# Kernel tuning notes

Hardware: AMD Instinct MI355X
Metric: run time of the kernel (lower is better)

The kernel has to match this reference:

```python
import jax, jax.numpy as jnp
import numpy as np

H = 16        # query heads
KV = 4        # key/value heads
HD = 64       # head dim
BASE = 10000.0
SCALE = HD ** (-0.5) * 0.8


def setup_inputs() -> dict:
    key = jax.random.key(0)
    ks = jax.random.split(key, 5)
    B, S, D = 2, 4096, 1024
    return {
        "hidden_states": jax.random.normal(ks[0], (B, S, D), dtype=jnp.float32),
        "wq": jax.random.normal(ks[1], (D, H * HD), dtype=jnp.float32) * (D ** -0.5),
        "wk": jax.random.normal(ks[2], (D, KV * HD), dtype=jnp.float32) * (D ** -0.5),
        "wv": jax.random.normal(ks[3], (D, KV * HD), dtype=jnp.float32) * (D ** -0.5),
        "wo": jax.random.normal(ks[4], (H * HD, D), dtype=jnp.float32) * ((H * HD) ** -0.5),
    }


def _rope_tables(seq_len, dtype):
    inv_freq = 1.0 / (BASE ** (jnp.arange(0, HD, 2, dtype=jnp.float32) / HD))
    t = jnp.arange(seq_len, dtype=jnp.float32)
    freqs = t[:, None] * inv_freq[None, :]            # [S, HD/2]
    emb = jnp.concatenate([freqs, freqs], axis=-1)    # [S, HD]
    return jnp.cos(emb).astype(dtype), jnp.sin(emb).astype(dtype)


def _rotate_half(x):
    x1, x2 = x[..., : HD // 2], x[..., HD // 2 :]
    return jnp.concatenate([-x2, x1], axis=-1)


def reference(hidden_states, wq, wk, wv, wo):
    B, S, D = hidden_states.shape
    G = H // KV
    q = (hidden_states @ wq).reshape(B, S, H, HD).transpose(0, 2, 1, 3)   # [B,H,S,HD]
    k = (hidden_states @ wk).reshape(B, S, KV, HD).transpose(0, 2, 1, 3)  # [B,KV,S,HD]
    v = (hidden_states @ wv).reshape(B, S, KV, HD).transpose(0, 2, 1, 3)
    cos, sin = _rope_tables(S, q.dtype)               # [S,HD] each
    cos = cos[None, None]                             # [1,1,S,HD]
    sin = sin[None, None]
    q = q * cos + _rotate_half(q) * sin
    k = k * cos + _rotate_half(k) * sin
    k = jnp.repeat(k, G, axis=1)                      # [B,H,S,HD]
    v = jnp.repeat(v, G, axis=1)
    scores = jnp.einsum("bhqd,bhkd->bhqk", q, k) * SCALE
    probs = jax.nn.softmax(scores.astype(jnp.float32), axis=-1).astype(q.dtype)
    out = jnp.einsum("bhqk,bhkd->bhqd", probs, v)     # [B,H,S,HD]
    out = out.transpose(0, 2, 1, 3).reshape(B, S, H * HD)
    return out @ wo
```

## Files before the change

### kernel.cpp

```cpp
#include <hip/hip_runtime.h>
#include <hip/hip_fp16.h>
#include <math.h>

typedef _Float16 f16;
typedef _Float16 half8 __attribute__((ext_vector_type(8)));
typedef _Float16 half4v __attribute__((ext_vector_type(4)));
typedef _Float16 half2v __attribute__((ext_vector_type(2)));
typedef float f32x4 __attribute__((ext_vector_type(4)));
typedef float f32x16 __attribute__((ext_vector_type(16)));
typedef unsigned uint2v __attribute__((ext_vector_type(2)));

#define NB 2
#define NS 4096
#define ND 1024
#define NH 16
#define NKV 4
#define NHD 64
#define ATT_SCALE2 0.14426950408889634f

__global__ __launch_bounds__(256) void wprep_k(
    const float* __restrict__ wq, const float* __restrict__ wk,
    const float* __restrict__ wv, const float* __restrict__ wo,
    f16* __restrict__ Bt, f16* __restrict__ Wot)
{
  __shared__ f16 tile[64][72];
  int bx = blockIdx.x, by = blockIdx.y;
  const float* src; int ldn, colbase, nbase; f16* dst;
  if (bx < 24) {
    int n0 = bx * 64;
    if (n0 < 1024)      { src = wq; ldn = 1024; colbase = n0; }
    else if (n0 < 1280) { src = wk; ldn = 256;  colbase = n0 - 1024; }
    else                { src = wv; ldn = 256;  colbase = n0 - 1280; }
    dst = Bt; nbase = n0;
  } else {
    src = wo; ldn = 1024; colbase = (bx - 24) * 64; dst = Wot; nbase = (bx - 24) * 64;
  }
  int tid = threadIdx.x;
  int kr = tid >> 4;
  int nc = (tid & 15) * 4;
  #pragma unroll
  for (int i = 0; i < 4; ++i) {
    int k = by * 64 + kr + i * 16;
    float4 v = *reinterpret_cast<const float4*>(src + (size_t)k * ldn + colbase + nc);
    tile[nc + 0][kr + i * 16] = (f16)v.x;
    tile[nc + 1][kr + i * 16] = (f16)v.y;
    tile[nc + 2][kr + i * 16] = (f16)v.z;
    tile[nc + 3][kr + i * 16] = (f16)v.w;
  }
  __syncthreads();
  int nl = tid >> 2;
  int kb = (tid & 3) * 16;
  half8 a = *reinterpret_cast<const half8*>(&tile[nl][kb]);
  half8 b = *reinterpret_cast<const half8*>(&tile[nl][kb + 8]);
  f16* o = dst + (size_t)(nbase + nl) * 1024 + by * 64 + kb;
  *reinterpret_cast<half8*>(o) = a;
  *reinterpret_cast<half8*>(o + 8) = b;
}

template<int MODE>
__global__ __launch_bounds__(256) void gemm_k(
    const float* __restrict__ Af32, const f16* __restrict__ Af16,
    const f16* __restrict__ Bt,
    f16* __restrict__ q_h, f16* __restrict__ k_h, f16* __restrict__ vT_h,
    float* __restrict__ outp)
{
  __shared__ f16 As[128 * 32];
  __shared__ f16 Bs[128 * 32];
  int tid = threadIdx.x;
  int lane = tid & 63, w = tid >> 6;
  int wr = w >> 1, wc = w & 1;
  int g = lane >> 4, lr = lane & 15;
  int m0 = blockIdx.y * 128, n0 = blockIdx.x * 128;

  f32x4 acc[4][4] = {};

  int ar = tid >> 1;
  int ac = (tid & 1) * 16;

  for (int k0 = 0; k0 < ND; k0 += 32) {
    if (MODE == 0) {
      const float* Ap = Af32 + (size_t)(m0 + ar) * ND + k0 + ac;
      #pragma unroll
      for (int i = 0; i < 4; ++i) {
        float4 v = *reinterpret_cast<const float4*>(Ap + i * 4);
        int col = ac + i * 4;
        int slot = (col >> 3) ^ (ar & 3);
        half4v hv = { (f16)v.x, (f16)v.y, (f16)v.z, (f16)v.w };
        *reinterpret_cast<half4v*>(&As[ar * 32 + slot * 8 + (col & 7)]) = hv;
      }
    } else {
      const f16* Ap = Af16 + (size_t)(m0 + ar) * ND + k0 + ac;
      half8 v0 = *reinterpret_cast<const half8*>(Ap);
      half8 v1 = *reinterpret_cast<const half8*>(Ap + 8);
      int s0 = (ac >> 3) ^ (ar & 3);
      int s1 = ((ac >> 3) + 1) ^ (ar & 3);
      *reinterpret_cast<half8*>(&As[ar * 32 + s0 * 8]) = v0;
      *reinterpret_cast<half8*>(&As[ar * 32 + s1 * 8]) = v1;
    }
    {
      const f16* Bp = Bt + (size_t)(n0 + ar) * ND + k0 + ac;
      half8 v0 = *reinterpret_cast<const half8*>(Bp);
      half8 v1 = *reinterpret_cast<const half8*>(Bp + 8);
      int s0 = (ac >> 3) ^ (ar & 3);
      int s1 = ((ac >> 3) + 1) ^ (ar & 3);
      *reinterpret_cast<half8*>(&Bs[ar * 32 + s0 * 8]) = v0;
      *reinterpret_cast<half8*>(&Bs[ar * 32 + s1 * 8]) = v1;
    }
    __syncthreads();
    half8 af[4], bf[4];
    #pragma unroll
    for (int mt = 0; mt < 4; ++mt) {
      int row = wr * 64 + mt * 16 + lr;
      af[mt] = *reinterpret_cast<const half8*>(&As[row * 32 + (g ^ (row & 3)) * 8]);
    }
    #pragma unroll
    for (int nt = 0; nt < 4; ++nt) {
      int row = wc * 64 + nt * 16 + lr;
      bf[nt] = *reinterpret_cast<const half8*>(&Bs[row * 32 + (g ^ (row & 3)) * 8]);
    }
    #pragma unroll
    for (int mt = 0; mt < 4; ++mt)
      #pragma unroll
      for (int nt = 0; nt < 4; ++nt)
        acc[mt][nt] = __builtin_amdgcn_mfma_f32_16x16x32_f16(af[mt], bf[nt], acc[mt][nt], 0, 0, 0);
    __syncthreads();
  }

  #pragma unroll
  for (int mt = 0; mt < 4; ++mt)
    #pragma unroll
    for (int nt = 0; nt < 4; ++nt)
      #pragma unroll
      for (int r = 0; r < 4; ++r) {
        int m = m0 + wr * 64 + mt * 16 + g * 4 + r;
        int n = n0 + wc * 64 + nt * 16 + lr;
        float val = acc[mt][nt][r];
        if (MODE == 0) {
          int b = m >> 12, s = m & (NS - 1);
          f16 hv = (f16)val;
          if (n < 1024)      q_h[(((size_t)b * NH + (n >> 6)) * NS + s) * NHD + (n & 63)] = hv;
          else if (n < 1280) { int nn = n - 1024; k_h[(((size_t)b * NKV + (nn >> 6)) * NS + s) * NHD + (nn & 63)] = hv; }
          else               { int nn = n - 1280; vT_h[(((size_t)b * NKV + (nn >> 6)) * NHD + (nn & 63)) * NS + s] = hv; }
        } else {
          outp[(size_t)m * ND + n] = val;
        }
      }
}

__global__ __launch_bounds__(256) void rope_k(f16* __restrict__ q_h, f16* __restrict__ k_h)
{
  __shared__ float cs[16][33], sn[16][33];
  int b = blockIdx.y;
  int s0 = blockIdx.x * 16;
  int tid = threadIdx.x;
  for (int idx = tid; idx < 512; idx += 256) {
    int sl = idx >> 5, d = idx & 31;
    double inv = exp((double)d * -0.28782313662425575);
    double ang = (double)(s0 + sl) * inv;
    cs[sl][d] = (float)cos(ang);
    sn[sl][d] = (float)sin(ang);
  }
  __syncthreads();
  for (int p = tid; p < 512 * 20; p += 256) {
    int u = p >> 9; int rem = p & 511; int sl = rem >> 5; int d = rem & 31;
    f16* ptr;
    if (u < NH) ptr = q_h + (((size_t)b * NH + u) * NS + s0 + sl) * NHD;
    else        ptr = k_h + (((size_t)b * NKV + (u - NH)) * NS + s0 + sl) * NHD;
    float x1 = (float)ptr[d], x2 = (float)ptr[d + 32];
    float c = cs[sl][d], si = sn[sl][d];
    ptr[d]      = (f16)(x1 * c - x2 * si);
    ptr[d + 32] = (f16)(x2 * c + x1 * si);
  }
}

__global__ __launch_bounds__(512) void attn_k(
    const f16* __restrict__ q_h, const f16* __restrict__ k_h,
    const f16* __restrict__ vT_h, f16* __restrict__ attn_h)
{
  __shared__ f16 Ks[2][64 * 64];
  __shared__ f16 Vs[2][64 * 64];
  int tid = threadIdx.x;
  int lane = tid & 63, w = tid >> 6;
  int hi = lane >> 5, qr = lane & 31;
  int bh = blockIdx.x; int b = bh >> 4, h = bh & 15, kvh = h >> 2;
  int q0 = blockIdx.y * 256 + w * 32;

  const f16* qptr = q_h + (((size_t)b * NH + h) * NS + q0 + qr) * NHD + hi * 8;
  half8 qf[4];
  #pragma unroll
  for (int ks = 0; ks < 4; ++ks)
    qf[ks] = *reinterpret_cast<const half8*>(qptr + 16 * ks);

  const f16* kbase = k_h + ((size_t)b * NKV + kvh) * NS * NHD;
  const f16* vbase = vT_h + ((size_t)b * NKV + kvh) * NHD * NS;

  f32x16 accO[2] = {};
  float m_run = -1e30f;
  float l_lane = 0.f;

  int srow = tid >> 3;
  int scol = (tid & 7) * 8;
  int sslot = ((scol >> 3) ^ (srow & 7)) * 8;
  int qs = qr & 7;

  {
    half8 kv0 = *reinterpret_cast<const half8*>(kbase + (size_t)srow * NHD + scol);
    half8 vv0 = *reinterpret_cast<const half8*>(vbase + (size_t)srow * NS + scol);
    *reinterpret_cast<half8*>(&Ks[0][srow * 64 + sslot]) = kv0;
    *reinterpret_cast<half8*>(&Vs[0][srow * 64 + sslot]) = vv0;
  }

  const half2v ones2 = { (f16)1.0f, (f16)1.0f };

  int cur = 0;
  for (int t = 0; t < 64; ++t) {
    __syncthreads();
    int tn = (t < 63) ? t + 1 : t;
    int kt2 = tn * 64;
    half8 kreg = *reinterpret_cast<const half8*>(kbase + (size_t)(kt2 + srow) * NHD + scol);
    half8 vreg = *reinterpret_cast<const half8*>(vbase + (size_t)srow * NS + kt2 + scol);

    const f16* Kc = &Ks[cur][0];
    const f16* Vc = &Vs[cur][0];

    f32x16 sc0 = {}, sc1 = {};
    #pragma unroll
    for (int ks = 0; ks < 4; ++ks) {
      int cs = 2 * ks + hi;
      half8 kf0 = *reinterpret_cast<const half8*>(&Kc[qr * 64 + ((cs ^ qs) << 3)]);
      half8 kf1 = *reinterpret_cast<const half8*>(&Kc[(32 + qr) * 64 + ((cs ^ qs) << 3)]);
      __builtin_amdgcn_s_setprio(1);
      sc0 = __builtin_amdgcn_mfma_f32_32x32x16_f16(kf0, qf[ks], sc0, 0, 0, 0);
      sc1 = __builtin_amdgcn_mfma_f32_32x32x16_f16(kf1, qf[ks], sc1, 0, 0, 0);
      __builtin_amdgcn_s_setprio(0);
    }

    float mx = sc0[0];
    #pragma unroll
    for (int i = 1; i < 16; ++i) mx = fmaxf(mx, sc0[i]);
    #pragma unroll
    for (int i = 0; i < 16; ++i) mx = fmaxf(mx, sc1[i]);
    float mxs = mx * ATT_SCALE2;

    if (__any(mxs > m_run + 8.0f)) {
      float mw = fmaxf(mxs, __shfl_xor(mxs, 32));
      float mnew = fmaxf(m_run, mw);
      float alpha = exp2f(m_run - mnew);
      #pragma unroll
      for (int db = 0; db < 2; ++db)
        #pragma unroll
        for (int i = 0; i < 16; ++i) accO[db][i] *= alpha;
      l_lane *= alpha;
      m_run = mnew;
    }

    unsigned wrd[2][4][2];
    float l0 = 0.f, l1 = 0.f;
    #pragma unroll
    for (int e = 0; e < 4; ++e)
      #pragma unroll
      for (int p = 0; p < 2; ++p) {
        float a0 = exp2f(fmaf(sc0[e * 4 + p * 2], ATT_SCALE2, -m_run));
        float a1 = exp2f(fmaf(sc0[e * 4 + p * 2 + 1], ATT_SCALE2, -m_run));
        unsigned u0 = __builtin_bit_cast(unsigned, __builtin_amdgcn_cvt_pkrtz(a0, a1));
        wrd[0][e][p] = u0;
        l0 = __builtin_amdgcn_fdot2(__builtin_bit_cast(half2v, u0), ones2, l0, false);
        float b0 = exp2f(fmaf(sc1[e * 4 + p * 2], ATT_SCALE2, -m_run));
        float b1 = exp2f(fmaf(sc1[e * 4 + p * 2 + 1], ATT_SCALE2, -m_run));
        unsigned u1 = __builtin_bit_cast(unsigned, __builtin_amdgcn_cvt_pkrtz(b0, b1));
        wrd[1][e][p] = u1;
        l1 = __builtin_amdgcn_fdot2(__builtin_bit_cast(half2v, u1), ones2, l1, false);
      }
    l_lane += l0 + l1;

    #pragma unroll
    for (int ks = 0; ks < 4; ++ks) {
      int kb = ks >> 1, e0 = 2 * (ks & 1);
      uint2v s0 = __builtin_amdgcn_permlane32_swap(wrd[kb][e0][0], wrd[kb][e0 + 1][0], false, false);
      uint2v s1 = __builtin_amdgcn_permlane32_swap(wrd[kb][e0][1], wrd[kb][e0 + 1][1], false, false);
      union { unsigned u[4]; half8 h; } pfu;
      pfu.u[0] = s0[0]; pfu.u[1] = s1[0]; pfu.u[2] = s0[1]; pfu.u[3] = s1[1];
      int cs = 2 * ks + hi;
      half8 vf0 = *reinterpret_cast<const half8*>(&Vc[qr * 64 + ((cs ^ qs) << 3)]);
      half8 vf1 = *reinterpret_cast<const half8*>(&Vc[(32 + qr) * 64 + ((cs ^ qs) << 3)]);
      __builtin_amdgcn_s_setprio(1);
      accO[0] = __builtin_amdgcn_mfma_f32_32x32x16_f16(vf0, pfu.h, accO[0], 0, 0, 0);
      accO[1] = __builtin_amdgcn_mfma_f32_32x32x16_f16(vf1, pfu.h, accO[1], 0, 0, 0);
      __builtin_amdgcn_s_setprio(0);
    }

    *reinterpret_cast<half8*>(&Ks[cur ^ 1][srow * 64 + sslot]) = kreg;
    *reinterpret_cast<half8*>(&Vs[cur ^ 1][srow * 64 + sslot]) = vreg;
    cur ^= 1;
  }

  float l_tot = l_lane + __shfl_xor(l_lane, 32);
  float inv_l = 1.0f / l_tot;
  f16* obase = attn_h + ((size_t)b * NS + q0 + qr) * ND + h * NHD;
  #pragma unroll
  for (int db = 0; db < 2; ++db)
    #pragma unroll
    for (int e = 0; e < 4; ++e) {
      half4v ov = { (f16)(accO[db][e * 4 + 0] * inv_l), (f16)(accO[db][e * 4 + 1] * inv_l),
                    (f16)(accO[db][e * 4 + 2] * inv_l), (f16)(accO[db][e * 4 + 3] * inv_l) };
      *reinterpret_cast<half4v*>(obase + db * 32 + e * 8 + hi * 4) = ov;
    }
}

extern "C" void kernel_launch(void* const* d_in, const int* in_sizes, int n_in,
                              void* d_out, int out_size, void* d_ws, size_t ws_size,
                              hipStream_t stream)
{
  (void)in_sizes; (void)n_in; (void)out_size; (void)ws_size;
  const float* hs = (const float*)d_in[0];
  const float* wq = (const float*)d_in[1];
  const float* wk = (const float*)d_in[2];
  const float* wv = (const float*)d_in[3];
  const float* wo = (const float*)d_in[4];
  float* outp = (float*)d_out;

  f16* q_h    = (f16*)d_ws;
  f16* k_h    = q_h    + (size_t)NB * NH * NS * NHD;
  f16* vT_h   = k_h    + (size_t)NB * NKV * NS * NHD;
  f16* attn_h = vT_h   + (size_t)NB * NKV * NS * NHD;
  f16* Bt     = attn_h + (size_t)NB * NS * ND;
  f16* Wot    = Bt     + (size_t)1536 * 1024;

  wprep_k<<<dim3(40, 16), 256, 0, stream>>>(wq, wk, wv, wo, Bt, Wot);
  gemm_k<0><<<dim3(12, 64), 256, 0, stream>>>(hs, nullptr, Bt, q_h, k_h, vT_h, nullptr);
  rope_k<<<dim3(256, 2), 256, 0, stream>>>(q_h, k_h);
  attn_k<<<dim3(32, 16), 512, 0, stream>>>(q_h, k_h, vT_h, attn_h);
  gemm_k<1><<<dim3(8, 64), 256, 0, stream>>>(nullptr, attn_h, Wot, nullptr, nullptr, nullptr, outp);
}
```

Baseline: 330.7 us.

## Fold softmax scale into Q and running max into MFMA accumulator init

The softmax scale (with log2e) is now applied to Q when the projection writes it, so the scores come out already scaled. The running max is kept as a negative offset vector (mtup) that seeds the first QK^T MFMA accumulator, so the per-element fma before each exp2 disappears. When a rescale is needed, the offset is subtracted from the scores and from mtup. The max reduction is also rewritten as a three-input max tree to allow max3 instructions. This trades per-element VALU work for storing a slightly larger-magnitude Q in fp16 and adding a few extra subtractions on the rescale path.

```diff
diff --git a/kernel.cpp b/kernel.cpp
--- a/kernel.cpp
+++ b/kernel.cpp
@@ -137,10 +137,11 @@
         float val = acc[mt][nt][r];
         if (MODE == 0) {
           int b = m >> 12, s = m & (NS - 1);
-          f16 hv = (f16)val;
-          if (n < 1024)      q_h[(((size_t)b * NH + (n >> 6)) * NS + s) * NHD + (n & 63)] = hv;
-          else if (n < 1280) { int nn = n - 1024; k_h[(((size_t)b * NKV + (nn >> 6)) * NS + s) * NHD + (nn & 63)] = hv; }
-          else               { int nn = n - 1280; vT_h[(((size_t)b * NKV + (nn >> 6)) * NHD + (nn & 63)) * NS + s] = hv; }
+          if (n < 1024) {
+            q_h[(((size_t)b * NH + (n >> 6)) * NS + s) * NHD + (n & 63)] = (f16)(val * ATT_SCALE2);
+          }
+          else if (n < 1280) { int nn = n - 1024; k_h[(((size_t)b * NKV + (nn >> 6)) * NS + s) * NHD + (nn & 63)] = (f16)val; }
+          else               { int nn = n - 1280; vT_h[(((size_t)b * NKV + (nn >> 6)) * NHD + (nn & 63)) * NS + s] = (f16)val; }
         } else {
           outp[(size_t)m * ND + n] = val;
         }
@@ -195,7 +196,7 @@
   const f16* vbase = vT_h + ((size_t)b * NKV + kvh) * NHD * NS;
 
   f32x16 accO[2] = {};
-  float m_run = -1e30f;
+  f32x16 mtup = {};
   float l_lane = 0.f;
 
   int srow = tid >> 3;
@@ -223,9 +224,17 @@
     const f16* Kc = &Ks[cur][0];
     const f16* Vc = &Vs[cur][0];
 
-    f32x16 sc0 = {}, sc1 = {};
-    #pragma unroll
-    for (int ks = 0; ks < 4; ++ks) {
+    f32x16 sc0, sc1;
+    {
+      half8 kf0 = *reinterpret_cast<const half8*>(&Kc[qr * 64 + ((hi ^ qs) << 3)]);
+      half8 kf1 = *reinterpret_cast<const half8*>(&Kc[(32 + qr) * 64 + ((hi ^ qs) << 3)]);
+      __builtin_amdgcn_s_setprio(1);
+      sc0 = __builtin_amdgcn_mfma_f32_32x32x16_f16(kf0, qf[0], mtup, 0, 0, 0);
+      sc1 = __builtin_amdgcn_mfma_f32_32x32x16_f16(kf1, qf[0], mtup, 0, 0, 0);
+      __builtin_amdgcn_s_setprio(0);
+    }
+    #pragma unroll
+    for (int ks = 1; ks < 4; ++ks) {
       int cs = 2 * ks + hi;
       half8 kf0 = *reinterpret_cast<const half8*>(&Kc[qr * 64 + ((cs ^ qs) << 3)]);
       half8 kf1 = *reinterpret_cast<const half8*>(&Kc[(32 + qr) * 64 + ((cs ^ qs) << 3)]);
@@ -235,23 +244,35 @@
       __builtin_amdgcn_s_setprio(0);
     }
 
-    float mx = sc0[0];
-    #pragma unroll
-    for (int i = 1; i < 16; ++i) mx = fmaxf(mx, sc0[i]);
-    #pragma unroll
-    for (int i = 0; i < 16; ++i) mx = fmaxf(mx, sc1[i]);
-    float mxs = mx * ATT_SCALE2;
-
-    if (__any(mxs > m_run + 8.0f)) {
-      float mw = fmaxf(mxs, __shfl_xor(mxs, 32));
-      float mnew = fmaxf(m_run, mw);
-      float alpha = exp2f(m_run - mnew);
+    #define MAX3F(a, b, c) fmaxf(fmaxf((a), (b)), (c))
+    float v0 = MAX3F(sc0[0],  sc0[1],  sc0[2]);
+    float v1 = MAX3F(sc0[3],  sc0[4],  sc0[5]);
+    float v2 = MAX3F(sc0[6],  sc0[7],  sc0[8]);
+    float v3 = MAX3F(sc0[9],  sc0[10], sc0[11]);
+    float v4 = MAX3F(sc0[12], sc0[13], sc0[14]);
+    float v5 = MAX3F(sc1[0],  sc1[1],  sc1[2]);
+    float v6 = MAX3F(sc1[3],  sc1[4],  sc1[5]);
+    float v7 = MAX3F(sc1[6],  sc1[7],  sc1[8]);
+    float v8 = MAX3F(sc1[9],  sc1[10], sc1[11]);
+    float v9 = MAX3F(sc1[12], sc1[13], sc1[14]);
+    float w0 = MAX3F(v0, v1, v2);
+    float w1 = MAX3F(v3, v4, sc0[15]);
+    float w2 = MAX3F(v5, v6, v7);
+    float w3 = MAX3F(v8, v9, sc1[15]);
+    float mx = fmaxf(MAX3F(w0, w1, w2), w3);
+    #undef MAX3F
+
+    if (__any(mx > 8.0f)) {
+      float mw = fmaxf(mx, __shfl_xor(mx, 32));
+      float r  = fmaxf(mw, 0.0f);
+      float alpha = exp2f(-r);
       #pragma unroll
       for (int db = 0; db < 2; ++db)
         #pragma unroll
         for (int i = 0; i < 16; ++i) accO[db][i] *= alpha;
       l_lane *= alpha;
-      m_run = mnew;
+      #pragma unroll
+      for (int i = 0; i < 16; ++i) { sc0[i] -= r; sc1[i] -= r; mtup[i] -= r; }
     }
 
     unsigned wrd[2][4][2];
@@ -260,13 +281,13 @@
     for (int e = 0; e < 4; ++e)
       #pragma unroll
       for (int p = 0; p < 2; ++p) {
-        float a0 = exp2f(fmaf(sc0[e * 4 + p * 2], ATT_SCALE2, -m_run));
-        float a1 = exp2f(fmaf(sc0[e * 4 + p * 2 + 1], ATT_SCALE2, -m_run));
+        float a0 = exp2f(sc0[e * 4 + p * 2]);
+        float a1 = exp2f(sc0[e * 4 + p * 2 + 1]);
         unsigned u0 = __builtin_bit_cast(unsigned, __builtin_amdgcn_cvt_pkrtz(a0, a1));
         wrd[0][e][p] = u0;
         l0 = __builtin_amdgcn_fdot2(__builtin_bit_cast(half2v, u0), ones2, l0, false);
-        float b0 = exp2f(fmaf(sc1[e * 4 + p * 2], ATT_SCALE2, -m_run));
-        float b1 = exp2f(fmaf(sc1[e * 4 + p * 2 + 1], ATT_SCALE2, -m_run));
+        float b0 = exp2f(sc1[e * 4 + p * 2]);
+        float b1 = exp2f(sc1[e * 4 + p * 2 + 1]);
         unsigned u1 = __builtin_bit_cast(unsigned, __builtin_amdgcn_cvt_pkrtz(b0, b1));
         wrd[1][e][p] = u1;
         l1 = __builtin_amdgcn_fdot2(__builtin_bit_cast(half2v, u1), ones2, l1, false);
```

After: 330.7 us. No clear change (-0.0%).

## Compute softmax exponentials speculatively and recompute the running max only on overflow

Applied to the files above, without the earlier changes.

The attention loop no longer reduces the row maximum on every tile. It exponentiates scores against the current running max, which now starts at 0, and tests whether any lane's tile sum exceeds a threshold. Only then does it compute the max with a max3 tree, rescale the accumulators and redo the exponentials. The scale-and-shift now uses packed f32x2 FMAs, and the row-sum is split across several accumulators. This cuts per-tile VALU work in the common case. In exchange, tiles that trigger the check pay for the exponentials twice, and rows whose scores sit well below zero may lose fp16 precision or underflow.

```diff
diff --git a/kernel.cpp b/kernel.cpp
--- a/kernel.cpp
+++ b/kernel.cpp
@@ -6,6 +6,7 @@
 typedef _Float16 half8 __attribute__((ext_vector_type(8)));
 typedef _Float16 half4v __attribute__((ext_vector_type(4)));
 typedef _Float16 half2v __attribute__((ext_vector_type(2)));
+typedef float f32x2 __attribute__((ext_vector_type(2)));
 typedef float f32x4 __attribute__((ext_vector_type(4)));
 typedef float f32x16 __attribute__((ext_vector_type(16)));
 typedef unsigned uint2v __attribute__((ext_vector_type(2)));
@@ -195,7 +196,7 @@
   const f16* vbase = vT_h + ((size_t)b * NKV + kvh) * NHD * NS;
 
   f32x16 accO[2] = {};
-  float m_run = -1e30f;
+  float m_run = 0.0f;
   float l_lane = 0.f;
 
   int srow = tid >> 3;
@@ -235,14 +236,57 @@
       __builtin_amdgcn_s_setprio(0);
     }
 
-    float mx = sc0[0];
-    #pragma unroll
-    for (int i = 1; i < 16; ++i) mx = fmaxf(mx, sc0[i]);
-    #pragma unroll
-    for (int i = 0; i < 16; ++i) mx = fmaxf(mx, sc1[i]);
-    float mxs = mx * ATT_SCALE2;
-
-    if (__any(mxs > m_run + 8.0f)) {
+    unsigned wrd[2][4][2];
+    float la0, la1, lb0, lb1;
+    auto pack_all = [&]() {
+      const f32x2 s2v = { ATT_SCALE2, ATT_SCALE2 };
+      const f32x2 nm2 = { -m_run, -m_run };
+      la0 = 0.f; la1 = 0.f; lb0 = 0.f; lb1 = 0.f;
+      #pragma unroll
+      for (int e = 0; e < 4; ++e)
+        #pragma unroll
+        for (int p = 0; p < 2; ++p) {
+          f32x2 a = { sc0[e * 4 + p * 2], sc0[e * 4 + p * 2 + 1] };
+          a = __builtin_elementwise_fma(a, s2v, nm2);
+          unsigned u0 = __builtin_bit_cast(unsigned,
+              __builtin_amdgcn_cvt_pkrtz(exp2f(a[0]), exp2f(a[1])));
+          wrd[0][e][p] = u0;
+          f32x2 bv = { sc1[e * 4 + p * 2], sc1[e * 4 + p * 2 + 1] };
+          bv = __builtin_elementwise_fma(bv, s2v, nm2);
+          unsigned u1 = __builtin_bit_cast(unsigned,
+              __builtin_amdgcn_cvt_pkrtz(exp2f(bv[0]), exp2f(bv[1])));
+          wrd[1][e][p] = u1;
+          if (e & 1) {
+            la1 = __builtin_amdgcn_fdot2(__builtin_bit_cast(half2v, u0), ones2, la1, false);
+            lb1 = __builtin_amdgcn_fdot2(__builtin_bit_cast(half2v, u1), ones2, lb1, false);
+          } else {
+            la0 = __builtin_amdgcn_fdot2(__builtin_bit_cast(half2v, u0), ones2, la0, false);
+            lb0 = __builtin_amdgcn_fdot2(__builtin_bit_cast(half2v, u1), ones2, lb0, false);
+          }
+        }
+    };
+    pack_all();
+    float ltile = (la0 + la1) + (lb0 + lb1);
+
+    if (__any(ltile > 8192.0f)) {
+      #define MAX3F(a, b, c) fmaxf(fmaxf((a), (b)), (c))
+      float v0 = MAX3F(sc0[0],  sc0[1],  sc0[2]);
+      float v1 = MAX3F(sc0[3],  sc0[4],  sc0[5]);
+      float v2 = MAX3F(sc0[6],  sc0[7],  sc0[8]);
+      float v3 = MAX3F(sc0[9],  sc0[10], sc0[11]);
+      float v4 = MAX3F(sc0[12], sc0[13], sc0[14]);
+      float v5 = MAX3F(sc1[0],  sc1[1],  sc1[2]);
+      float v6 = MAX3F(sc1[3],  sc1[4],  sc1[5]);
+      float v7 = MAX3F(sc1[6],  sc1[7],  sc1[8]);
+      float v8 = MAX3F(sc1[9],  sc1[10], sc1[11]);
+      float v9 = MAX3F(sc1[12], sc1[13], sc1[14]);
+      float w0 = MAX3F(v0, v1, v2);
+      float w1 = MAX3F(v3, v4, sc0[15]);
+      float w2 = MAX3F(v5, v6, v7);
+      float w3 = MAX3F(v8, v9, sc1[15]);
+      float mx = fmaxf(MAX3F(w0, w1, w2), w3);
+      #undef MAX3F
+      float mxs = mx * ATT_SCALE2;
       float mw = fmaxf(mxs, __shfl_xor(mxs, 32));
       float mnew = fmaxf(m_run, mw);
       float alpha = exp2f(m_run - mnew);
@@ -252,26 +296,10 @@
         for (int i = 0; i < 16; ++i) accO[db][i] *= alpha;
       l_lane *= alpha;
       m_run = mnew;
-    }
-
-    unsigned wrd[2][4][2];
-    float l0 = 0.f, l1 = 0.f;
-    #pragma unroll
-    for (int e = 0; e < 4; ++e)
-      #pragma unroll
-      for (int p = 0; p < 2; ++p) {
-        float a0 = exp2f(fmaf(sc0[e * 4 + p * 2], ATT_SCALE2, -m_run));
-        float a1 = exp2f(fmaf(sc0[e * 4 + p * 2 + 1], ATT_SCALE2, -m_run));
-        unsigned u0 = __builtin_bit_cast(unsigned, __builtin_amdgcn_cvt_pkrtz(a0, a1));
-        wrd[0][e][p] = u0;
-        l0 = __builtin_amdgcn_fdot2(__builtin_bit_cast(half2v, u0), ones2, l0, false);
-        float b0 = exp2f(fmaf(sc1[e * 4 + p * 2], ATT_SCALE2, -m_run));
-        float b1 = exp2f(fmaf(sc1[e * 4 + p * 2 + 1], ATT_SCALE2, -m_run));
-        unsigned u1 = __builtin_bit_cast(unsigned, __builtin_amdgcn_cvt_pkrtz(b0, b1));
-        wrd[1][e][p] = u1;
-        l1 = __builtin_amdgcn_fdot2(__builtin_bit_cast(half2v, u1), ones2, l1, false);
-      }
-    l_lane += l0 + l1;
+      pack_all();
+      ltile = (la0 + la1) + (lb0 + lb1);
+    }
+    l_lane += ltile;
 
     #pragma unroll
     for (int ks = 0; ks < 4; ++ks) {
```

Result: slower. 344.7 us (+4.2%).
